# Performance work log

Measured on AMD Instinct MI355X. Metric: run time of the kernel, lower is better.

Reference implementation:

```python
import jax, jax.numpy as jnp
import numpy as np

D = 768
H = 12
B, T = 2, 2048


def _layernorm(x, g, b, eps=1e-5):
    m = jnp.mean(x, axis=-1, keepdims=True)
    v = jnp.mean((x - m) ** 2, axis=-1, keepdims=True)
    return (x - m) * jax.lax.rsqrt(v + eps) * g + b


def setup_inputs() -> dict:
    key = jax.random.key(0)
    ks = jax.random.split(key, 10)
    s = 0.02
    return {
        "x": jax.random.normal(ks[0], (B, T, D), dtype=jnp.float32),
        "attn_mask": jnp.ones((B, T), dtype=jnp.int32),
        "Wq": jax.random.normal(ks[1], (D, D), dtype=jnp.float32) * s,
        "Wk": jax.random.normal(ks[2], (D, D), dtype=jnp.float32) * s,
        "Wv": jax.random.normal(ks[3], (D, D), dtype=jnp.float32) * s,
        "Wo": jax.random.normal(ks[4], (D, D), dtype=jnp.float32) * s,
        "bo": jnp.zeros((D,), dtype=jnp.float32),
        "ln1_g": jnp.ones((D,), dtype=jnp.float32),
        "ln1_b": jnp.zeros((D,), dtype=jnp.float32),
        "ln2_g": jnp.ones((D,), dtype=jnp.float32),
        "ln2_b": jnp.zeros((D,), dtype=jnp.float32),
        "W1": jax.random.normal(ks[5], (D, 4 * D), dtype=jnp.float32) * s,
        "b1": jnp.zeros((4 * D,), dtype=jnp.float32),
        "W2": jax.random.normal(ks[6], (4 * D, D), dtype=jnp.float32) * s,
        "b2": jnp.zeros((D,), dtype=jnp.float32),
    }


def reference(x, attn_mask, Wq, Wk, Wv, Wo, bo, ln1_g, ln1_b, ln2_g, ln2_b, W1, b1, W2, b2):
    d = x.shape[-1]
    hs = d // H
    # --- multi-head self-attention on ln1(x) ---
    h = _layernorm(x, ln1_g, ln1_b)
    q = jnp.einsum("btd,dhk->bhtk", h, Wq.reshape(d, H, hs))
    k = jnp.einsum("btd,dhk->bhtk", h, Wk.reshape(d, H, hs))
    v = jnp.einsum("btd,dhk->bhtk", h, Wv.reshape(d, H, hs))
    # NOTE: original scales by embed_dim**-0.5 (C = embed_dim), not head_size
    scores = jnp.einsum("bhtk,bhsk->bhts", q, k) * (d ** -0.5)
    key_mask = (attn_mask == 0)[:, None, None, :]  # [B,1,1,T] over key dim
    scores = jnp.where(key_mask, -jnp.inf, scores)
    wei = jax.nn.softmax(scores, axis=-1)
    out = jnp.einsum("bhts,bhsk->bhtk", wei, v)
    out = out.transpose(0, 2, 1, 3).reshape(x.shape)  # concat heads -> [B,T,D]
    x = x + out @ Wo + bo
    # --- feed-forward on ln2(x) ---
    h2 = _layernorm(x, ln2_g, ln2_b)
    ff = jax.nn.relu(h2 @ W1 + b1) @ W2 + b2
    return x + ff
```

## Files before the change

### kernel.cpp

```cpp
#include <hip/hip_runtime.h>
#include <hip/hip_bf16.h>


typedef unsigned short u16;
typedef unsigned int u32;
typedef __attribute__((ext_vector_type(8))) short s16x8;
typedef __attribute__((ext_vector_type(4))) short s16x4;
typedef __attribute__((ext_vector_type(4))) float fx4;

#define D_MODEL 768
#define NH 12
#define HS 64
#define TT 2048
#define BB 2

__device__ __forceinline__ u16 f2bf(float f) {
  union { float f; u32 u; } v; v.f = f;
  u32 r = v.u + 0x7fffu + ((v.u >> 16) & 1u);
  return (u16)(r >> 16);
}
__device__ __forceinline__ float bf2f(u16 h) {
  union { u32 u; float f; } v; v.u = ((u32)h) << 16; return v.f;
}
__device__ __forceinline__ s16x4 pack4(float a, float b, float c, float d) {
  union { __hip_bfloat162 h2[2]; s16x4 v; } u;
  u.h2[0] = __float22bfloat162_rn({a, b});
  u.h2[1] = __float22bfloat162_rn({c, d});
  return u.v;
}

__device__ __forceinline__ void async16(const void* g, void* l) {
  __builtin_amdgcn_global_load_lds(
      (const __attribute__((address_space(1))) u32*)g,
      (__attribute__((address_space(3))) u32*)l, 16, 0, 0);
}

__global__ __launch_bounds__(256) void preproc(
    const float* __restrict__ x, const int* __restrict__ mask,
    const float* __restrict__ Wq, const float* __restrict__ Wk,
    const float* __restrict__ Wv, const float* __restrict__ Wo,
    const float* __restrict__ W1, const float* __restrict__ W2,
    const float* __restrict__ g1, const float* __restrict__ be1,
    u16* __restrict__ WqkvT, u16* __restrict__ WoT,
    u16* __restrict__ W1T, u16* __restrict__ W2T,
    u16* __restrict__ h1, u16* __restrict__ mb) {
  __shared__ float t[32][33];
  __shared__ float ss[4], ssq[4];
  const int bid = blockIdx.x, tid = threadIdx.x;
  if (bid < 6912) {
    const float* in; u16* out; int R, C, cx, cy;
    if (bid < 1728) {
      int wsel = bid / 576, s = bid % 576;
      in = wsel == 0 ? Wq : wsel == 1 ? Wk : Wv;
      out = WqkvT + (size_t)wsel * 768 * 768;
      R = 768; C = 768; cx = s % 24; cy = s / 24;
    } else if (bid < 2304) {
      int s = bid - 1728; in = Wo; out = WoT;
      R = 768; C = 768; cx = s % 24; cy = s / 24;
    } else if (bid < 4608) {
      int s = bid - 2304; in = W1; out = W1T;
      R = 768; C = 3072; cx = s % 96; cy = s / 96;
    } else {
      int s = bid - 4608; in = W2; out = W2T;
      R = 3072; C = 768; cx = s % 24; cy = s / 24;
    }
    int c0 = cx * 32, r0 = cy * 32, xx = tid & 31, yy = tid >> 5;
    for (int i = 0; i < 4; i++)
      t[yy + i * 8][xx] = in[(size_t)(r0 + yy + i * 8) * C + c0 + xx];
    __syncthreads();
    for (int i = 0; i < 4; i++)
      out[(size_t)(c0 + yy + i * 8) * R + r0 + xx] = f2bf(t[xx][yy + i * 8]);
  } else if (bid < 11008) {
    int row = bid - 6912;
    const float* xr = x + (size_t)row * D_MODEL;
    float v0 = xr[tid], v1 = xr[tid + 256], v2 = xr[tid + 512];
    float s = v0 + v1 + v2, sq = v0 * v0 + v1 * v1 + v2 * v2;
    for (int m = 1; m < 64; m <<= 1) { s += __shfl_xor(s, m); sq += __shfl_xor(sq, m); }
    int w = tid >> 6;
    if ((tid & 63) == 0) { ss[w] = s; ssq[w] = sq; }
    __syncthreads();
    s = ss[0] + ss[1] + ss[2] + ss[3];
    sq = ssq[0] + ssq[1] + ssq[2] + ssq[3];
    float mean = s * (1.f / D_MODEL);
    float var = sq * (1.f / D_MODEL) - mean * mean;
    float rstd = rsqrtf(var + 1e-5f);
    u16* orow = h1 + (size_t)row * D_MODEL;
    orow[tid]       = f2bf((v0 - mean) * rstd * g1[tid]       + be1[tid]);
    orow[tid + 256] = f2bf((v1 - mean) * rstd * g1[tid + 256] + be1[tid + 256]);
    orow[tid + 512] = f2bf((v2 - mean) * rstd * g1[tid + 512] + be1[tid + 512]);
  } else {
    int i = (bid - 11008) * 256 + tid;
    mb[i] = mask[i] ? (u16)0 : f2bf(-1e30f);
  }
}

__global__ __launch_bounds__(256) void red_wo_ln(
    const u16* __restrict__ p0, const u16* __restrict__ p1,
    const float* __restrict__ x, const float* __restrict__ bo,
    const float* __restrict__ g, const float* __restrict__ be,
    float* __restrict__ yv, u16* __restrict__ h2) {
  int row = blockIdx.x, tid = threadIdx.x;
  size_t base = (size_t)row * D_MODEL;
  float v[3];
  float s = 0.f, sq = 0.f;
  for (int i = 0; i < 3; i++) {
    int c = tid + i * 256;
    size_t idx = base + c;
    float t = bf2f(p0[idx]) + bf2f(p1[idx]) + x[idx] + bo[c];
    v[i] = t; yv[idx] = t;
    s += t; sq += t * t;
  }
  for (int m = 1; m < 64; m <<= 1) { s += __shfl_xor(s, m); sq += __shfl_xor(sq, m); }
  __shared__ float ss[4], ssq[4];
  int w = tid >> 6;
  if ((tid & 63) == 0) { ss[w] = s; ssq[w] = sq; }
  __syncthreads();
  s = ss[0] + ss[1] + ss[2] + ss[3];
  sq = ssq[0] + ssq[1] + ssq[2] + ssq[3];
  float mean = s * (1.f / D_MODEL);
  float var = sq * (1.f / D_MODEL) - mean * mean;
  float rstd = rsqrtf(var + 1e-5f);
  for (int i = 0; i < 3; i++) {
    int c = tid + i * 256;
    h2[base + c] = f2bf((v[i] - mean) * rstd * g[c] + be[c]);
  }
}

__global__ __launch_bounds__(256) void red_ff2(
    const u16* __restrict__ p0, const u16* __restrict__ p1,
    const float* __restrict__ yv,
    const float* __restrict__ bias, float* __restrict__ out) {
  size_t i = ((size_t)blockIdx.x * 256 + threadIdx.x) * 4;
  int col = (int)(i % D_MODEL);
  ushort4 a = *(const ushort4*)(p0 + i);
  ushort4 b = *(const ushort4*)(p1 + i);
  float4 y = *(const float4*)(yv + i);
  float4 o;
  o.x = bf2f(a.x) + bf2f(b.x) + y.x + bias[col];
  o.y = bf2f(a.y) + bf2f(b.y) + y.y + bias[col + 1];
  o.z = bf2f(a.z) + bf2f(b.z) + y.z + bias[col + 2];
  o.w = bf2f(a.w) + bf2f(b.w) + y.w + bias[col + 3];
  *(float4*)(out + i) = o;
}

template <int EPI>
__global__ __launch_bounds__(256) void gemm_bt(
    const u16* __restrict__ A, const u16* __restrict__ Bt,
    int M, int N, int K,
    u16* __restrict__ outb, const float* __restrict__ bias,
    float qs, u16* __restrict__ vtp,
    u16* __restrict__ p0, u16* __restrict__ p1) {
  __shared__ __align__(16) u16 lA[64 * 64];
  __shared__ __align__(16) u16 lB[128 * 64];
  const int tid = threadIdx.x;
  const int lane = tid & 63, w = tid >> 6;
  const int quad = lane >> 4, l15 = lane & 15;
  const int wm = w >> 1, wn = w & 1;
  const int bm = blockIdx.y, bn = blockIdx.x;
  const int Ksub = K / gridDim.z;
  const int k0 = blockIdx.z * Ksub;

  fx4 acc[2][4] = {};

  for (int kt = k0; kt < k0 + Ksub; kt += 64) {
    __syncthreads();
    #pragma unroll
    for (int t = 0; t < 2; t++) {
      int p = t * 256 + tid;
      int m = p >> 3, qp = p & 7, ql = qp ^ (m & 7);
      async16(A + (size_t)(bm * 64 + m) * K + kt + ql * 8,
              (char*)lA + t * 4096 + w * 1024);
    }
    #pragma unroll
    for (int t = 0; t < 4; t++) {
      int p = t * 256 + tid;
      int n = p >> 3, qp = p & 7, ql = qp ^ (n & 7);
      async16(Bt + (size_t)(bn * 128 + n) * K + kt + ql * 8,
              (char*)lB + t * 4096 + w * 1024);
    }
    __syncthreads();
    #pragma unroll
    for (int kk = 0; kk < 2; kk++) {
      s16x8 af[2], bfr[4];
      #pragma unroll
      for (int i = 0; i < 2; i++) {
        int m = wm * 32 + i * 16 + l15;
        af[i] = *(const s16x8*)((const char*)lA + m * 128 +
                                (((kk * 4 + quad) ^ (m & 7)) * 16));
      }
      #pragma unroll
      for (int j = 0; j < 4; j++) {
        int n = wn * 64 + j * 16 + l15;
        bfr[j] = *(const s16x8*)((const char*)lB + n * 128 +
                                 (((kk * 4 + quad) ^ (n & 7)) * 16));
      }
      #pragma unroll
      for (int i = 0; i < 2; i++)
        #pragma unroll
        for (int j = 0; j < 4; j++)
          acc[i][j] = __builtin_amdgcn_mfma_f32_16x16x32_bf16(af[i], bfr[j], acc[i][j], 0, 0, 0);
    }
  }

  u16* pb = (EPI == 3) ? (blockIdx.z == 0 ? p0 : p1) : nullptr;

  #pragma unroll
  for (int i = 0; i < 2; i++)
    #pragma unroll
    for (int j = 0; j < 4; j++) {
      int row0 = bm * 64 + wm * 32 + i * 16 + quad * 4;
      int col = bn * 128 + wn * 64 + j * 16 + l15;
      if (EPI == 0) {
        if (vtp != nullptr && col >= 1536) {
          int bb = row0 >> 11, t0 = row0 & 2047;
          ushort4 pk = {f2bf(acc[i][j][0]), f2bf(acc[i][j][1]),
                        f2bf(acc[i][j][2]), f2bf(acc[i][j][3])};
          *(ushort4*)(vtp + ((size_t)(bb * 768 + (col - 1536)) << 11) + t0) = pk;
        } else {
          float sc = (col < 768) ? qs : 1.f;
          for (int r = 0; r < 4; r++)
            outb[(size_t)(row0 + r) * N + col] = f2bf(acc[i][j][r] * sc);
        }
      } else if (EPI == 2) {
        for (int r = 0; r < 4; r++)
          outb[(size_t)(row0 + r) * N + col] = f2bf(fmaxf(acc[i][j][r] + bias[col], 0.f));
      } else {
        for (int r = 0; r < 4; r++)
          pb[(size_t)(row0 + r) * N + col] = f2bf(acc[i][j][r]);
      }
    }
}

__global__ __launch_bounds__(256) void attn_kernel(
    const u16* __restrict__ qkv, const u16* __restrict__ vt,
    const u16* __restrict__ maskadd, u16* __restrict__ out) {
  __shared__ __align__(16) u16 sQ[64 * 64];
  __shared__ __align__(16) u16 sK[64 * 64];
  __shared__ __align__(16) u16 sV[64 * 68];
  __shared__ __align__(16) u16 smask[2048];
  const int bh = blockIdx.y, b = bh / NH, h = bh % NH;
  const int qt = blockIdx.x;
  const int tid = threadIdx.x, lane = tid & 63, w = tid >> 6;
  const int quad = lane >> 4, l15 = lane & 15;

  #pragma unroll
  for (int i = 0; i < 2; i++) {
    int p = i * 256 + tid;
    int m = p >> 3, qp = p & 7, ql = qp ^ (m & 7);
    async16(qkv + (size_t)(b * TT + qt * 64 + m) * 2304 + h * HS + ql * 8,
            (char*)sQ + i * 4096 + w * 1024);
  }
  #pragma unroll
  for (int j = 0; j < 8; j++)
    smask[j * 256 + tid] = maskadd[b * TT + j * 256 + tid];
  const int vr = tid >> 3, vc = tid & 7;
  const u16* vb0 = vt + ((size_t)bh * HS + vr) * TT;
  const u16* vb1 = vt + ((size_t)bh * HS + vr + 32) * TT;
  s16x8 vcur0 = *(const s16x8*)(vb0 + vc * 8);
  s16x8 vcur1 = *(const s16x8*)(vb1 + vc * 8);
  __syncthreads();

  const int qrow = w * 16 + l15;
  s16x8 aq0 = *(const s16x8*)((const char*)sQ + qrow * 128 + ((quad ^ (l15 & 7)) * 16));
  s16x8 aq1 = *(const s16x8*)((const char*)sQ + qrow * 128 + (((4 + quad) ^ (l15 & 7)) * 16));

  const char* pK0 = (const char*)sK + l15 * 128 + ((quad ^ (l15 & 7)) * 16);
  const char* pK1 = (const char*)sK + l15 * 128 + (((4 + quad) ^ (l15 & 7)) * 16);
  const char* pV  = (const char*)sV + l15 * 136 + quad * 8;
  char* vw0 = (char*)sV + vr * 136 + vc * 16;
  char* vw1 = vw0 + 32 * 136;

  float lsum = 0.f;
  fx4 o[4] = {};

  for (int kc = 0; kc < 32; kc++) {
    __syncthreads();
    #pragma unroll
    for (int i = 0; i < 2; i++) {
      int p = i * 256 + tid;
      int m = p >> 3, qp = p & 7, ql = qp ^ (m & 7);
      async16(qkv + (size_t)(b * TT + kc * 64 + m) * 2304 + D_MODEL + h * HS + ql * 8,
              (char*)sK + i * 4096 + w * 1024);
    }
    *(s16x8*)vw0 = vcur0;
    *(s16x8*)vw1 = vcur1;
    __syncthreads();
    int kn = (kc < 31 ? kc + 1 : kc) * 64;
    s16x8 vn0 = *(const s16x8*)(vb0 + kn + vc * 8);
    s16x8 vn1 = *(const s16x8*)(vb1 + kn + vc * 8);

    #pragma unroll
    for (int kt = 0; kt < 4; kt++) {
      ushort4 mk = *(const ushort4*)&smask[kc * 64 + kt * 16 + quad * 4];
      fx4 s = {bf2f(mk.x), bf2f(mk.y), bf2f(mk.z), bf2f(mk.w)};
      s16x8 ak0 = *(const s16x8*)(pK0 + kt * 2048);
      s16x8 ak1 = *(const s16x8*)(pK1 + kt * 2048);
      s = __builtin_amdgcn_mfma_f32_16x16x32_bf16(ak0, aq0, s, 0, 0, 0);
      s = __builtin_amdgcn_mfma_f32_16x16x32_bf16(ak1, aq1, s, 0, 0, 0);
      float e0 = __builtin_amdgcn_exp2f(s[0]);
      float e1 = __builtin_amdgcn_exp2f(s[1]);
      float e2 = __builtin_amdgcn_exp2f(s[2]);
      float e3 = __builtin_amdgcn_exp2f(s[3]);
      lsum += (e0 + e1) + (e2 + e3);
      s16x4 pB = pack4(e0, e1, e2, e3);
      #pragma unroll
      for (int jv = 0; jv < 4; jv++) {
        s16x4 av = *(const s16x4*)(pV + jv * 2176 + kt * 32);
        o[jv] = __builtin_amdgcn_mfma_f32_16x16x16bf16_1k(av, pB, o[jv], 0, 0, 0);
      }
    }
    vcur0 = vn0; vcur1 = vn1;
  }

  lsum += __shfl_xor(lsum, 16);
  lsum += __shfl_xor(lsum, 32);
  float rinv = 1.f / lsum;

  __syncthreads();
  u16* sT = sV;
  #pragma unroll
  for (int jv = 0; jv < 4; jv++)
    #pragma unroll
    for (int r = 0; r < 4; r++) {
      int vd = jv * 16 + quad * 4 + r;
      sT[vd * 68 + w * 16 + l15] = f2bf(o[jv][r] * rinv);
    }
  __syncthreads();
  int q = tid >> 2, c = tid & 3;
  u16* orow = out + (size_t)(b * TT + qt * 64 + q) * D_MODEL + h * HS + c * 16;
  s16x8 o0, o1;
  #pragma unroll
  for (int i = 0; i < 8; i++) o0[i] = (short)sT[(c * 16 + i) * 68 + q];
  #pragma unroll
  for (int i = 0; i < 8; i++) o1[i] = (short)sT[(c * 16 + 8 + i) * 68 + q];
  *(s16x8*)orow = o0;
  *(s16x8*)(orow + 8) = o1;
}

extern "C" void kernel_launch(void* const* d_in, const int* in_sizes, int n_in,
                              void* d_out, int out_size, void* d_ws, size_t ws_size,
                              hipStream_t stream) {
  const float* x    = (const float*)d_in[0];
  const int*   mask = (const int*)d_in[1];
  const float* Wq   = (const float*)d_in[2];
  const float* Wk   = (const float*)d_in[3];
  const float* Wv   = (const float*)d_in[4];
  const float* Wo   = (const float*)d_in[5];
  const float* bo   = (const float*)d_in[6];
  const float* g1   = (const float*)d_in[7];
  const float* be1  = (const float*)d_in[8];
  const float* g2   = (const float*)d_in[9];
  const float* be2  = (const float*)d_in[10];
  const float* W1   = (const float*)d_in[11];
  const float* bb1  = (const float*)d_in[12];
  const float* W2   = (const float*)d_in[13];
  const float* bb2  = (const float*)d_in[14];
  float* out = (float*)d_out;
  char* ws = (char*)d_ws;

  u16*   WqkvT = (u16*)(ws + 0);
  u16*   WoT   = (u16*)(ws + 3538944);
  u16*   W1T   = (u16*)(ws + 4718592);
  u16*   W2T   = (u16*)(ws + 9437184);
  u16*   h1    = (u16*)(ws + 14155776);
  u16*   QKV   = (u16*)(ws + 20447232);
  u16*   Vt    = (u16*)(ws + 39321600);
  u16*   attn  = (u16*)(ws + 45613056);
  float* yv    = (float*)(ws + 51904512);
  u16*   mbias = (u16*)(ws + 51904512);
  u16*   h2    = h1;
  u16*   ff1   = QKV;
  u16* pw0 = (u16*)(ws + 20447232);
  u16* pw1 = (u16*)(ws + 26738688);
  u16* pf0 = (u16*)(ws + 0);
  u16* pf1 = (u16*)(ws + 14155776);

  const float QS = 0.05205875399f;

  preproc<<<11024, 256, 0, stream>>>(x, mask, Wq, Wk, Wv, Wo, W1, W2,
                                     g1, be1, WqkvT, WoT, W1T, W2T, h1, mbias);
  gemm_bt<0><<<dim3(18, 64, 1), 256, 0, stream>>>(h1, WqkvT, 4096, 2304, 768,
      QKV, nullptr, QS, Vt, nullptr, nullptr);
  attn_kernel<<<dim3(32, 24), 256, 0, stream>>>(QKV, Vt, mbias, attn);
  gemm_bt<3><<<dim3(6, 64, 2), 256, 0, stream>>>(attn, WoT, 4096, 768, 768,
      nullptr, nullptr, 1.f, nullptr, pw0, pw1);
  red_wo_ln<<<4096, 256, 0, stream>>>(pw0, pw1, x, bo, g2, be2, yv, h2);
  gemm_bt<2><<<dim3(24, 64, 1), 256, 0, stream>>>(h2, W1T, 4096, 3072, 768,
      ff1, bb1, 1.f, nullptr, nullptr, nullptr);
  gemm_bt<3><<<dim3(6, 64, 2), 256, 0, stream>>>(ff1, W2T, 4096, 768, 3072,
      nullptr, nullptr, 1.f, nullptr, pf0, pf1);
  red_ff2<<<3072, 256, 0, stream>>>(pf0, pf1, yv, bb2, out);
}
```

Measured before the change: 284.7 us.

## Split attention key range across two wave groups per block

The attention kernel now uses 512 threads. Two groups of four waves each process half of the 2048 keys, with separate K/V shared buffers. Their unnormalized outputs and row sums are combined through shared memory before normalization and the store. This doubles the waves working on each query tile and halves the serial key loop, at the cost of more shared memory and an extra reduction step.

```diff
diff --git a/kernel.cpp b/kernel.cpp
--- a/kernel.cpp
+++ b/kernel.cpp
@@ -231,67 +231,67 @@
     }
 }
 
-__global__ __launch_bounds__(256) void attn_kernel(
+__global__ __launch_bounds__(512) void attn_kernel(
     const u16* __restrict__ qkv, const u16* __restrict__ vt,
     const u16* __restrict__ maskadd, u16* __restrict__ out) {
   __shared__ __align__(16) u16 sQ[64 * 64];
-  __shared__ __align__(16) u16 sK[64 * 64];
-  __shared__ __align__(16) u16 sV[64 * 68];
+  __shared__ __align__(16) u16 sK[2][64 * 64];
+  __shared__ __align__(16) u16 sV[2][64 * 68];
   __shared__ __align__(16) u16 smask[2048];
+  __shared__ float sL[64];
   const int bh = blockIdx.y, b = bh / NH, h = bh % NH;
   const int qt = blockIdx.x;
   const int tid = threadIdx.x, lane = tid & 63, w = tid >> 6;
   const int quad = lane >> 4, l15 = lane & 15;
-
+  const int g = w >> 2, wg = w & 3, gtid = tid & 255;
+
+  {
+    int m = tid >> 3, qp = tid & 7, ql = qp ^ (m & 7);
+    async16(qkv + (size_t)(b * TT + qt * 64 + m) * 2304 + h * HS + ql * 8,
+            (char*)sQ + w * 1024);
+  }
   #pragma unroll
-  for (int i = 0; i < 2; i++) {
-    int p = i * 256 + tid;
-    int m = p >> 3, qp = p & 7, ql = qp ^ (m & 7);
-    async16(qkv + (size_t)(b * TT + qt * 64 + m) * 2304 + h * HS + ql * 8,
-            (char*)sQ + i * 4096 + w * 1024);
-  }
-  #pragma unroll
-  for (int j = 0; j < 8; j++)
-    smask[j * 256 + tid] = maskadd[b * TT + j * 256 + tid];
-  const int vr = tid >> 3, vc = tid & 7;
-  const u16* vb0 = vt + ((size_t)bh * HS + vr) * TT;
-  const u16* vb1 = vt + ((size_t)bh * HS + vr + 32) * TT;
+  for (int j = 0; j < 4; j++)
+    smask[j * 512 + tid] = maskadd[b * TT + j * 512 + tid];
+  const int vr = gtid >> 3, vc = gtid & 7;
+  const u16* vb0 = vt + ((size_t)bh * HS + vr) * TT + g * 1024;
+  const u16* vb1 = vt + ((size_t)bh * HS + vr + 32) * TT + g * 1024;
   s16x8 vcur0 = *(const s16x8*)(vb0 + vc * 8);
   s16x8 vcur1 = *(const s16x8*)(vb1 + vc * 8);
   __syncthreads();
 
-  const int qrow = w * 16 + l15;
+  const int qrow = wg * 16 + l15;
   s16x8 aq0 = *(const s16x8*)((const char*)sQ + qrow * 128 + ((quad ^ (l15 & 7)) * 16));
   s16x8 aq1 = *(const s16x8*)((const char*)sQ + qrow * 128 + (((4 + quad) ^ (l15 & 7)) * 16));
 
-  const char* pK0 = (const char*)sK + l15 * 128 + ((quad ^ (l15 & 7)) * 16);
-  const char* pK1 = (const char*)sK + l15 * 128 + (((4 + quad) ^ (l15 & 7)) * 16);
-  const char* pV  = (const char*)sV + l15 * 136 + quad * 8;
-  char* vw0 = (char*)sV + vr * 136 + vc * 16;
+  const char* pK0 = (const char*)sK[g] + l15 * 128 + ((quad ^ (l15 & 7)) * 16);
+  const char* pK1 = (const char*)sK[g] + l15 * 128 + (((4 + quad) ^ (l15 & 7)) * 16);
+  const char* pV  = (const char*)sV[g] + l15 * 136 + quad * 8;
+  char* vw0 = (char*)sV[g] + vr * 136 + vc * 16;
   char* vw1 = vw0 + 32 * 136;
 
   float lsum = 0.f;
   fx4 o[4] = {};
 
-  for (int kc = 0; kc < 32; kc++) {
+  for (int kc = 0; kc < 16; kc++) {
     __syncthreads();
     #pragma unroll
     for (int i = 0; i < 2; i++) {
-      int p = i * 256 + tid;
+      int p = i * 256 + gtid;
       int m = p >> 3, qp = p & 7, ql = qp ^ (m & 7);
-      async16(qkv + (size_t)(b * TT + kc * 64 + m) * 2304 + D_MODEL + h * HS + ql * 8,
-              (char*)sK + i * 4096 + w * 1024);
+      async16(qkv + (size_t)(b * TT + g * 1024 + kc * 64 + m) * 2304 + D_MODEL + h * HS + ql * 8,
+              (char*)sK[g] + i * 4096 + wg * 1024);
     }
     *(s16x8*)vw0 = vcur0;
     *(s16x8*)vw1 = vcur1;
     __syncthreads();
-    int kn = (kc < 31 ? kc + 1 : kc) * 64;
+    int kn = (kc < 15 ? kc + 1 : kc) * 64;
     s16x8 vn0 = *(const s16x8*)(vb0 + kn + vc * 8);
     s16x8 vn1 = *(const s16x8*)(vb1 + kn + vc * 8);
 
     #pragma unroll
     for (int kt = 0; kt < 4; kt++) {
-      ushort4 mk = *(const ushort4*)&smask[kc * 64 + kt * 16 + quad * 4];
+      ushort4 mk = *(const ushort4*)&smask[g * 1024 + kc * 64 + kt * 16 + quad * 4];
       fx4 s = {bf2f(mk.x), bf2f(mk.y), bf2f(mk.z), bf2f(mk.w)};
       s16x8 ak0 = *(const s16x8*)(pK0 + kt * 2048);
       s16x8 ak1 = *(const s16x8*)(pK1 + kt * 2048);
@@ -314,27 +314,44 @@
 
   lsum += __shfl_xor(lsum, 16);
   lsum += __shfl_xor(lsum, 32);
-  float rinv = 1.f / lsum;
-
+
+  float* cbuf = (float*)sV;
+  u16*   sT   = (u16*)sK;
   __syncthreads();
-  u16* sT = sV;
-  #pragma unroll
-  for (int jv = 0; jv < 4; jv++)
-    #pragma unroll
-    for (int r = 0; r < 4; r++) {
-      int vd = jv * 16 + quad * 4 + r;
-      sT[vd * 68 + w * 16 + l15] = f2bf(o[jv][r] * rinv);
-    }
+  if (g == 1) {
+    #pragma unroll
+    for (int jv = 0; jv < 4; jv++)
+      #pragma unroll
+      for (int r = 0; r < 4; r++) {
+        int vd = jv * 16 + quad * 4 + r;
+        cbuf[vd * 66 + wg * 16 + l15] = o[jv][r];
+      }
+    if (quad == 0) sL[wg * 16 + l15] = lsum;
+  }
   __syncthreads();
-  int q = tid >> 2, c = tid & 3;
-  u16* orow = out + (size_t)(b * TT + qt * 64 + q) * D_MODEL + h * HS + c * 16;
-  s16x8 o0, o1;
-  #pragma unroll
-  for (int i = 0; i < 8; i++) o0[i] = (short)sT[(c * 16 + i) * 68 + q];
-  #pragma unroll
-  for (int i = 0; i < 8; i++) o1[i] = (short)sT[(c * 16 + 8 + i) * 68 + q];
-  *(s16x8*)orow = o0;
-  *(s16x8*)(orow + 8) = o1;
+  if (g == 0) {
+    float rinv = 1.f / (lsum + sL[wg * 16 + l15]);
+    #pragma unroll
+    for (int jv = 0; jv < 4; jv++)
+      #pragma unroll
+      for (int r = 0; r < 4; r++) {
+        int vd = jv * 16 + quad * 4 + r;
+        float v = o[jv][r] + cbuf[vd * 66 + wg * 16 + l15];
+        sT[vd * 68 + wg * 16 + l15] = f2bf(v * rinv);
+      }
+  }
+  __syncthreads();
+  if (tid < 256) {
+    int q = tid >> 2, c = tid & 3;
+    u16* orow = out + (size_t)(b * TT + qt * 64 + q) * D_MODEL + h * HS + c * 16;
+    s16x8 o0, o1;
+    #pragma unroll
+    for (int i = 0; i < 8; i++) o0[i] = (short)sT[(c * 16 + i) * 68 + q];
+    #pragma unroll
+    for (int i = 0; i < 8; i++) o1[i] = (short)sT[(c * 16 + 8 + i) * 68 + q];
+    *(s16x8*)orow = o0;
+    *(s16x8*)(orow + 8) = o1;
+  }
 }
 
 extern "C" void kernel_launch(void* const* d_in, const int* in_sizes, int n_in,
@@ -381,7 +398,7 @@
                                      g1, be1, WqkvT, WoT, W1T, W2T, h1, mbias);
   gemm_bt<0><<<dim3(18, 64, 1), 256, 0, stream>>>(h1, WqkvT, 4096, 2304, 768,
       QKV, nullptr, QS, Vt, nullptr, nullptr);
-  attn_kernel<<<dim3(32, 24), 256, 0, stream>>>(QKV, Vt, mbias, attn);
+  attn_kernel<<<dim3(32, 24), 512, 0, stream>>>(QKV, Vt, mbias, attn);
   gemm_bt<3><<<dim3(6, 64, 2), 256, 0, stream>>>(attn, WoT, 4096, 768, 768,
       nullptr, nullptr, 1.f, nullptr, pw0, pw1);
   red_wo_ln<<<4096, 256, 0, stream>>>(pw0, pw1, x, bo, g2, be2, yv, h2);
```

Result: no change. 279.3 us (-1.9%).
